# Kernel optimization log

Hardware: AMD Instinct MI355X
Metric: run time of the kernel (lower is better)

Reference implementation:

```python
import jax, jax.numpy as jnp
import numpy as np

N_ENTITIES = 100000
N_EDGES = 600000
N_RELATIONS = 24
D = 128


def setup_inputs() -> dict:
    key = jax.random.key(0)
    k1, k2, k3, k4 = jax.random.split(key, 4)
    ego_embed = jax.random.normal(k1, (N_ENTITIES, D), dtype=jnp.float32)
    edge_index = jax.random.randint(k2, (2, N_EDGES), 0, N_ENTITIES, dtype=jnp.int64)
    edge_type = jax.random.randint(k3, (N_EDGES,), 0, N_RELATIONS, dtype=jnp.int64)
    relation_weight = jax.random.normal(k4, (N_RELATIONS, D), dtype=jnp.float32)
    return {
        "ego_embed": ego_embed,
        "edge_index": edge_index,
        "edge_type": edge_type,
        "relation_weight": relation_weight,
    }


def reference(ego_embed, edge_index, edge_type, relation_weight):
    head, tail = edge_index[0], edge_index[1]
    n_entities = ego_embed.shape[0]
    # gather tail entity embeddings and relation embeddings, form messages
    msg = ego_embed[tail] * relation_weight[edge_type]  # [E, D]
    # scatter-mean aggregate messages per head entity
    agg = jax.ops.segment_sum(msg, head, num_segments=n_entities)  # [N, D]
    cnt = jax.ops.segment_sum(
        jnp.ones((msg.shape[0], 1), dtype=msg.dtype), head, num_segments=n_entities
    )  # [N, 1]
    entity_agg = agg / jnp.maximum(cnt, jnp.asarray(1, msg.dtype))
    return entity_agg
```

## Files before the change

### kernel.cpp

```cpp
#include <hip/hip_runtime.h>

#define D 128
#define CAP 32
#define SB 512
#define NREL 24
#define ABLOCKS 2048
#define CONVBLOCKS 2048

__device__ __forceinline__ unsigned short f2bf_rne(float f) {
    unsigned b = __float_as_uint(f);
    b += 0x7fffu + ((b >> 16) & 1u);
    return (unsigned short)(b >> 16);
}

__global__ void prep_k(const float* __restrict__ ego, ushort* __restrict__ egob, int n4,
                       const int* __restrict__ head, const int* __restrict__ tail,
                       const int* __restrict__ etype, int* __restrict__ cnt,
                       unsigned* __restrict__ csr, int nE) {
    int b = blockIdx.x;
    int tid = threadIdx.x;
    if (b < CONVBLOCKS) {
        const float4* __restrict__ in4 = (const float4*)ego;
        ushort4* __restrict__ o4 = (ushort4*)egob;
        int stride = CONVBLOCKS * 256;
        for (int i = b * 256 + tid; i < n4; i += stride) {
            float4 v = in4[i];
            ushort4 o;
            o.x = f2bf_rne(v.x); o.y = f2bf_rne(v.y);
            o.z = f2bf_rne(v.z); o.w = f2bf_rne(v.w);
            o4[i] = o;
        }
    } else {
        int i = (b - CONVBLOCKS) * 256 + tid;
        if (i < nE) {
            int h = head[i];
            int pos = atomicAdd(&cnt[h], 1);
            if (pos < CAP)
                csr[(size_t)h * CAP + pos] = ((unsigned)tail[i] << 5) | (unsigned)etype[i];
        }
    }
}

__global__ void __launch_bounds__(256, 8)
agg5_k(const ushort* __restrict__ egob, const float* __restrict__ relw,
       const unsigned* __restrict__ csr, const int* __restrict__ cnt,
       float* __restrict__ out, int nEnt) {
    __shared__ float4 lds4[NREL * 32];

    int tid = threadIdx.x;
    const float4* __restrict__ rw4 = (const float4*)relw;
    for (int i = tid; i < NREL * 32; i += 256) lds4[i] = rw4[i];
    __syncthreads();

    int gtid = blockIdx.x * 256 + tid;
    int w    = gtid >> 6;
    int lane = tid & 63;
    int half = lane >> 5;
    int l31  = lane & 31;

    int nwaves = (ABLOCKS * 256) >> 6;
    int chunk  = (nEnt + nwaves - 1) / nwaves;
    int e0 = w * chunk;
    int e1 = e0 + chunk; if (e1 > nEnt) e1 = nEnt;

    const uint2* __restrict__ eg2 = (const uint2*)egob;
    float4* __restrict__ out4 = (float4*)out;

    for (int ent = e0; ent < e1; ++ent) {
        int c = __builtin_amdgcn_readfirstlane(cnt[ent]);
        int m = (c < CAP) ? c : CAP;
        const unsigned* __restrict__ row = csr + (size_t)ent * CAP;

        float a0x = 0.f, a0y = 0.f, a0z = 0.f, a0w = 0.f;
        float a1x = 0.f, a1y = 0.f, a1z = 0.f, a1w = 0.f;

        for (int k = 0; k < m; k += 4) {
            uint4 q = *(const uint4*)(row + k);
            unsigned ua = half ? q.y : q.x;
            unsigned ub = half ? q.w : q.z;
            bool va = (k + half) < m;
            bool vb = (k + 2 + half) < m;
            if (va) {
                uint2 v = eg2[(int)(ua >> 5) * 32 + l31];
                float4 wv = lds4[(ua & 31u) * 32 + l31];
                a0x += __uint_as_float(v.x << 16)         * wv.x;
                a0y += __uint_as_float(v.x & 0xffff0000u) * wv.y;
                a0z += __uint_as_float(v.y << 16)         * wv.z;
                a0w += __uint_as_float(v.y & 0xffff0000u) * wv.w;
            }
            if (vb) {
                uint2 v = eg2[(int)(ub >> 5) * 32 + l31];
                float4 wv = lds4[(ub & 31u) * 32 + l31];
                a1x += __uint_as_float(v.x << 16)         * wv.x;
                a1y += __uint_as_float(v.x & 0xffff0000u) * wv.y;
                a1z += __uint_as_float(v.y << 16)         * wv.z;
                a1w += __uint_as_float(v.y & 0xffff0000u) * wv.w;
            }
        }
        float sx = a0x + a1x, sy = a0y + a1y, sz = a0z + a1z, sw = a0w + a1w;
        sx += __shfl_xor(sx, 32);
        sy += __shfl_xor(sy, 32);
        sz += __shfl_xor(sz, 32);
        sw += __shfl_xor(sw, 32);
        if (half == 0) {
            float inv = 1.0f / fmaxf((float)c, 1.0f);
            float4 o; o.x = sx * inv; o.y = sy * inv; o.z = sz * inv; o.w = sw * inv;
            out4[(size_t)ent * 32 + l31] = o;
        }
    }
}


__global__ void count_k(const int* __restrict__ head, int* __restrict__ counts, int nE) {
    int i = blockIdx.x * blockDim.x + threadIdx.x;
    if (i < nE) atomicAdd(&counts[head[i]], 1);
}

__global__ void blocksum_k(const int* __restrict__ counts, int* __restrict__ bsum, int nEnt) {
    __shared__ int s[SB];
    int t = threadIdx.x;
    int i = blockIdx.x * SB + t;
    s[t] = (i < nEnt) ? counts[i] : 0;
    __syncthreads();
    for (int off = SB / 2; off > 0; off >>= 1) {
        if (t < off) s[t] += s[t + off];
        __syncthreads();
    }
    if (t == 0) bsum[blockIdx.x] = s[0];
}

__global__ void scanb_k(int* __restrict__ bsum, int nSB) {
    __shared__ int s[SB];
    int t = threadIdx.x;
    int v = (t < nSB) ? bsum[t] : 0;
    s[t] = v;
    __syncthreads();
    for (int off = 1; off < SB; off <<= 1) {
        int x = (t >= off) ? s[t - off] : 0;
        __syncthreads();
        s[t] += x;
        __syncthreads();
    }
    if (t < nSB) bsum[t] = s[t] - v;
}

__global__ void writerows_k(const int* __restrict__ counts, const int* __restrict__ bsum,
                            int* __restrict__ rowstart, int* __restrict__ cursor, int nEnt) {
    __shared__ int s[SB];
    int t = threadIdx.x;
    int i = blockIdx.x * SB + t;
    int v = (i < nEnt) ? counts[i] : 0;
    s[t] = v;
    __syncthreads();
    for (int off = 1; off < SB; off <<= 1) {
        int x = (t >= off) ? s[t - off] : 0;
        __syncthreads();
        s[t] += x;
        __syncthreads();
    }
    if (i < nEnt) {
        int excl = s[t] - v + bsum[blockIdx.x];
        rowstart[i] = excl;
        cursor[i]   = excl;
    }
}

__global__ void bucket_k(const int* __restrict__ head, const int* __restrict__ tail,
                         const int* __restrict__ etype, int* __restrict__ cursor,
                         unsigned* __restrict__ csr, int nE) {
    int i = blockIdx.x * blockDim.x + threadIdx.x;
    if (i < nE) {
        int h = head[i];
        int pos = atomicAdd(&cursor[h], 1);
        csr[pos] = ((unsigned)tail[i] << 5) | (unsigned)etype[i];
    }
}

__global__ void agg_k(const float* __restrict__ ego, const float* __restrict__ relw,
                      const unsigned* __restrict__ csr, const int* __restrict__ rowstart,
                      const int* __restrict__ counts, float* __restrict__ out, int nEnt) {
    int gtid = blockIdx.x * blockDim.x + threadIdx.x;
    int wid  = gtid >> 6;
    int lane = gtid & 63;
    if (wid >= nEnt) return;
    int rs = __builtin_amdgcn_readfirstlane(rowstart[wid]);
    int c  = __builtin_amdgcn_readfirstlane(counts[wid]);
    const float2* __restrict__ ego2 = (const float2*)ego;
    const float2* __restrict__ rw2  = (const float2*)relw;
    float2 acc; acc.x = 0.f; acc.y = 0.f;
    unsigned u = (c > 0) ? csr[rs] : 0u;
    for (int k = 0; k < c; ++k) {
        unsigned un = (k + 1 < c) ? csr[rs + k + 1] : 0u;
        int t = (int)(u >> 5);
        int r = (int)(u & 31u);
        float2 v = ego2[(size_t)t * 64 + lane];
        float2 w = rw2[(size_t)r * 64 + lane];
        acc.x += v.x * w.x;
        acc.y += v.y * w.y;
        u = un;
    }
    float inv = 1.0f / fmaxf((float)c, 1.0f);
    float2 o; o.x = acc.x * inv; o.y = acc.y * inv;
    ((float2*)out)[(size_t)wid * 64 + lane] = o;
}

extern "C" void kernel_launch(void* const* d_in, const int* in_sizes, int n_in,
                              void* d_out, int out_size, void* d_ws, size_t ws_size,
                              hipStream_t stream) {
    const float* ego   = (const float*)d_in[0];
    const int*   eidx  = (const int*)d_in[1];
    const int*   etype = (const int*)d_in[2];
    const float* relw  = (const float*)d_in[3];
    float* out = (float*)d_out;

    int nE   = in_sizes[2];
    int nEnt = in_sizes[0] / D;
    const int* head = eidx;
    const int* tail = eidx + nE;

    char* ws = (char*)d_ws;
    size_t cntB  = (size_t)nEnt * 4;
    size_t csrB  = (size_t)nEnt * CAP * 4;
    size_t egoB  = (size_t)nEnt * D * 2;
    size_t needFast = cntB + csrB + egoB;

    int EB = (nE + 255) / 256;

    if (ws_size >= needFast) {
        int*      cnt  = (int*)ws;
        unsigned* csr  = (unsigned*)(ws + cntB);
        ushort*   egob = (ushort*)(ws + cntB + csrB);

        hipMemsetAsync(cnt, 0, cntB, stream);
        int n4 = nEnt * D / 4;
        prep_k<<<CONVBLOCKS + EB, 256, 0, stream>>>(ego, egob, n4,
                                                    head, tail, etype, cnt, csr, nE);
        agg5_k<<<ABLOCKS, 256, 0, stream>>>(egob, relw, csr, cnt, out, nEnt);
    } else {
        int nSB = (nEnt + SB - 1) / SB;
        int*      counts   = (int*)ws;
        int*      rowstart = (int*)(ws + cntB);
        int*      cursor   = (int*)(ws + cntB * 2);
        int*      bsum     = (int*)(ws + cntB * 3);
        unsigned* csr      = (unsigned*)(ws + cntB * 3 + SB * 4);

        int ablocks = (int)(((size_t)nEnt * 64 + 255) / 256);
        hipMemsetAsync(counts, 0, cntB, stream);
        count_k<<<EB, 256, 0, stream>>>(head, counts, nE);
        blocksum_k<<<nSB, SB, 0, stream>>>(counts, bsum, nEnt);
        scanb_k<<<1, SB, 0, stream>>>(bsum, nSB);
        writerows_k<<<nSB, SB, 0, stream>>>(counts, bsum, rowstart, cursor, nEnt);
        bucket_k<<<EB, 256, 0, stream>>>(head, tail, etype, cursor, csr, nE);
        agg_k<<<ablocks, 256, 0, stream>>>(ego, relw, csr, rowstart, counts, out, nEnt);
    }
}
```

Before: 100.1 us.

## Interleave prep work across all blocks and widen aggregation to full-wave rows

The prep kernel now uses a grid-stride loop in every block, and odd and even blocks run the CSR build and the bf16 conversion in opposite orders, so atomics and streaming conversion overlap instead of running in separate block ranges. The aggregation kernel has all 64 lanes cover one 128-wide row with 2 floats per lane, rather than two half-waves taking alternate edges. It issues 8 independent gathers per iteration to raise memory-level parallelism and drops the cross-half shuffle reduction. The costs are more registers per thread, narrower 4-byte gather loads, and weight reads from LDS for padded slots beyond the edge count.

```diff
diff --git a/kernel.cpp b/kernel.cpp
--- a/kernel.cpp
+++ b/kernel.cpp
@@ -5,7 +5,7 @@
 #define SB 512
 #define NREL 24
 #define ABLOCKS 2048
-#define CONVBLOCKS 2048
+#define PBLOCKS 4096
 
 __device__ __forceinline__ unsigned short f2bf_rne(float f) {
     unsigned b = __float_as_uint(f);
@@ -13,100 +13,116 @@
     return (unsigned short)(b >> 16);
 }
 
-__global__ void prep_k(const float* __restrict__ ego, ushort* __restrict__ egob, int n4,
-                       const int* __restrict__ head, const int* __restrict__ tail,
-                       const int* __restrict__ etype, int* __restrict__ cnt,
-                       unsigned* __restrict__ csr, int nE) {
-    int b = blockIdx.x;
-    int tid = threadIdx.x;
-    if (b < CONVBLOCKS) {
-        const float4* __restrict__ in4 = (const float4*)ego;
-        ushort4* __restrict__ o4 = (ushort4*)egob;
-        int stride = CONVBLOCKS * 256;
-        for (int i = b * 256 + tid; i < n4; i += stride) {
-            float4 v = in4[i];
-            ushort4 o;
-            o.x = f2bf_rne(v.x); o.y = f2bf_rne(v.y);
-            o.z = f2bf_rne(v.z); o.w = f2bf_rne(v.w);
-            o4[i] = o;
-        }
+
+__device__ __forceinline__ void conv_slice(const float* __restrict__ ego,
+                                           ushort* __restrict__ egob, int n4,
+                                           int g, int stride) {
+    const float4* __restrict__ in4 = (const float4*)ego;
+    ushort4* __restrict__ o4 = (ushort4*)egob;
+    for (int i = g; i < n4; i += stride) {
+        float4 v = in4[i];
+        ushort4 o;
+        o.x = f2bf_rne(v.x); o.y = f2bf_rne(v.y);
+        o.z = f2bf_rne(v.z); o.w = f2bf_rne(v.w);
+        o4[i] = o;
+    }
+}
+
+__device__ __forceinline__ void build_slice(const int* __restrict__ head,
+                                            const int* __restrict__ tail,
+                                            const int* __restrict__ etype,
+                                            int* __restrict__ cnt,
+                                            unsigned* __restrict__ csr,
+                                            int nE, int g, int stride) {
+    for (int i = g; i < nE; i += stride) {
+        int h = head[i];
+        int pos = atomicAdd(&cnt[h], 1);
+        if (pos < CAP)
+            csr[(size_t)h * CAP + pos] = ((unsigned)tail[i] << 5) | (unsigned)etype[i];
+    }
+}
+
+__global__ void fused_prep_k(const float* __restrict__ ego, ushort* __restrict__ egob, int n4,
+                             const int* __restrict__ head, const int* __restrict__ tail,
+                             const int* __restrict__ etype, int* __restrict__ cnt,
+                             unsigned* __restrict__ csr, int nE) {
+    int g = blockIdx.x * blockDim.x + threadIdx.x;
+    int stride = gridDim.x * blockDim.x;
+    if (blockIdx.x & 1) {
+        build_slice(head, tail, etype, cnt, csr, nE, g, stride);
+        conv_slice(ego, egob, n4, g, stride);
     } else {
-        int i = (b - CONVBLOCKS) * 256 + tid;
-        if (i < nE) {
-            int h = head[i];
-            int pos = atomicAdd(&cnt[h], 1);
-            if (pos < CAP)
-                csr[(size_t)h * CAP + pos] = ((unsigned)tail[i] << 5) | (unsigned)etype[i];
-        }
+        conv_slice(ego, egob, n4, g, stride);
+        build_slice(head, tail, etype, cnt, csr, nE, g, stride);
     }
 }
 
 __global__ void __launch_bounds__(256, 8)
-agg5_k(const ushort* __restrict__ egob, const float* __restrict__ relw,
+agg6_k(const ushort* __restrict__ egob, const float* __restrict__ relw,
        const unsigned* __restrict__ csr, const int* __restrict__ cnt,
        float* __restrict__ out, int nEnt) {
-    __shared__ float4 lds4[NREL * 32];
+    __shared__ float2 ldsw[32 * 64];
 
     int tid = threadIdx.x;
-    const float4* __restrict__ rw4 = (const float4*)relw;
-    for (int i = tid; i < NREL * 32; i += 256) lds4[i] = rw4[i];
+    const float2* __restrict__ rw2 = (const float2*)relw;
+    for (int i = tid; i < NREL * 64; i += 256) ldsw[i] = rw2[i];
     __syncthreads();
 
     int gtid = blockIdx.x * 256 + tid;
     int w    = gtid >> 6;
     int lane = tid & 63;
-    int half = lane >> 5;
-    int l31  = lane & 31;
 
     int nwaves = (ABLOCKS * 256) >> 6;
     int chunk  = (nEnt + nwaves - 1) / nwaves;
     int e0 = w * chunk;
     int e1 = e0 + chunk; if (e1 > nEnt) e1 = nEnt;
 
-    const uint2* __restrict__ eg2 = (const uint2*)egob;
-    float4* __restrict__ out4 = (float4*)out;
+    const unsigned* __restrict__ eg = (const unsigned*)egob;
+    float2* __restrict__ out2 = (float2*)out;
 
     for (int ent = e0; ent < e1; ++ent) {
         int c = __builtin_amdgcn_readfirstlane(cnt[ent]);
         int m = (c < CAP) ? c : CAP;
         const unsigned* __restrict__ row = csr + (size_t)ent * CAP;
 
-        float a0x = 0.f, a0y = 0.f, a0z = 0.f, a0w = 0.f;
-        float a1x = 0.f, a1y = 0.f, a1z = 0.f, a1w = 0.f;
-
-        for (int k = 0; k < m; k += 4) {
-            uint4 q = *(const uint4*)(row + k);
-            unsigned ua = half ? q.y : q.x;
-            unsigned ub = half ? q.w : q.z;
-            bool va = (k + half) < m;
-            bool vb = (k + 2 + half) < m;
-            if (va) {
-                uint2 v = eg2[(int)(ua >> 5) * 32 + l31];
-                float4 wv = lds4[(ua & 31u) * 32 + l31];
-                a0x += __uint_as_float(v.x << 16)         * wv.x;
-                a0y += __uint_as_float(v.x & 0xffff0000u) * wv.y;
-                a0z += __uint_as_float(v.y << 16)         * wv.z;
-                a0w += __uint_as_float(v.y & 0xffff0000u) * wv.w;
-            }
-            if (vb) {
-                uint2 v = eg2[(int)(ub >> 5) * 32 + l31];
-                float4 wv = lds4[(ub & 31u) * 32 + l31];
-                a1x += __uint_as_float(v.x << 16)         * wv.x;
-                a1y += __uint_as_float(v.x & 0xffff0000u) * wv.y;
-                a1z += __uint_as_float(v.y << 16)         * wv.z;
-                a1w += __uint_as_float(v.y & 0xffff0000u) * wv.w;
-            }
+        float ax = 0.f, ay = 0.f;
+
+        for (int k = 0; k < m; k += 8) {
+            uint4 q0 = *(const uint4*)(row + k);
+            uint4 q1 = *(const uint4*)(row + k + 4);
+
+            unsigned v0 = 0, v1 = 0, v2 = 0, v3 = 0, v4 = 0, v5 = 0, v6 = 0, v7 = 0;
+            if (k + 0 < m) v0 = eg[(size_t)(q0.x >> 5) * 64 + lane];
+            if (k + 1 < m) v1 = eg[(size_t)(q0.y >> 5) * 64 + lane];
+            if (k + 2 < m) v2 = eg[(size_t)(q0.z >> 5) * 64 + lane];
+            if (k + 3 < m) v3 = eg[(size_t)(q0.w >> 5) * 64 + lane];
+            if (k + 4 < m) v4 = eg[(size_t)(q1.x >> 5) * 64 + lane];
+            if (k + 5 < m) v5 = eg[(size_t)(q1.y >> 5) * 64 + lane];
+            if (k + 6 < m) v6 = eg[(size_t)(q1.z >> 5) * 64 + lane];
+            if (k + 7 < m) v7 = eg[(size_t)(q1.w >> 5) * 64 + lane];
+
+            float2 w0 = ldsw[(q0.x & 31u) * 64 + lane];
+            float2 w1 = ldsw[(q0.y & 31u) * 64 + lane];
+            float2 w2 = ldsw[(q0.z & 31u) * 64 + lane];
+            float2 w3 = ldsw[(q0.w & 31u) * 64 + lane];
+            float2 w4 = ldsw[(q1.x & 31u) * 64 + lane];
+            float2 w5 = ldsw[(q1.y & 31u) * 64 + lane];
+            float2 w6 = ldsw[(q1.z & 31u) * 64 + lane];
+            float2 w7 = ldsw[(q1.w & 31u) * 64 + lane];
+
+            ax += __uint_as_float(v0 << 16) * w0.x; ay += __uint_as_float(v0 & 0xffff0000u) * w0.y;
+            ax += __uint_as_float(v1 << 16) * w1.x; ay += __uint_as_float(v1 & 0xffff0000u) * w1.y;
+            ax += __uint_as_float(v2 << 16) * w2.x; ay += __uint_as_float(v2 & 0xffff0000u) * w2.y;
+            ax += __uint_as_float(v3 << 16) * w3.x; ay += __uint_as_float(v3 & 0xffff0000u) * w3.y;
+            ax += __uint_as_float(v4 << 16) * w4.x; ay += __uint_as_float(v4 & 0xffff0000u) * w4.y;
+            ax += __uint_as_float(v5 << 16) * w5.x; ay += __uint_as_float(v5 & 0xffff0000u) * w5.y;
+            ax += __uint_as_float(v6 << 16) * w6.x; ay += __uint_as_float(v6 & 0xffff0000u) * w6.y;
+            ax += __uint_as_float(v7 << 16) * w7.x; ay += __uint_as_float(v7 & 0xffff0000u) * w7.y;
         }
-        float sx = a0x + a1x, sy = a0y + a1y, sz = a0z + a1z, sw = a0w + a1w;
-        sx += __shfl_xor(sx, 32);
-        sy += __shfl_xor(sy, 32);
-        sz += __shfl_xor(sz, 32);
-        sw += __shfl_xor(sw, 32);
-        if (half == 0) {
-            float inv = 1.0f / fmaxf((float)c, 1.0f);
-            float4 o; o.x = sx * inv; o.y = sy * inv; o.z = sz * inv; o.w = sw * inv;
-            out4[(size_t)ent * 32 + l31] = o;
-        }
+
+        float inv = 1.0f / fmaxf((float)c, 1.0f);
+        float2 o; o.x = ax * inv; o.y = ay * inv;
+        out2[(size_t)ent * 64 + lane] = o;
     }
 }
 
@@ -233,9 +249,9 @@
 
         hipMemsetAsync(cnt, 0, cntB, stream);
         int n4 = nEnt * D / 4;
-        prep_k<<<CONVBLOCKS + EB, 256, 0, stream>>>(ego, egob, n4,
-                                                    head, tail, etype, cnt, csr, nE);
-        agg5_k<<<ABLOCKS, 256, 0, stream>>>(egob, relw, csr, cnt, out, nEnt);
+        fused_prep_k<<<PBLOCKS, 256, 0, stream>>>(ego, egob, n4,
+                                                  head, tail, etype, cnt, csr, nE);
+        agg6_k<<<ABLOCKS, 256, 0, stream>>>(egob, relw, csr, cnt, out, nEnt);
     } else {
         int nSB = (nEnt + SB - 1) / SB;
         int*      counts   = (int*)ws;
```

Result: faster. 87.44 us (-12.6%).
